# Optimization experiments

Hardware: AMD Instinct MI355X
Metric: run time of the kernel (lower is better)

## Reference

```python
import jax, jax.numpy as jnp
import numpy as np

D_MODEL = 1024
DEPTH = 1024

def setup_inputs() -> dict:
    key = jax.random.key(0)
    ks = jax.random.split(key, 7)
    scale = 1.0 / np.sqrt(D_MODEL)
    x = jax.random.normal(ks[0], (4, 2048, D_MODEL), dtype=jnp.float32)
    Wq = jax.random.normal(ks[1], (D_MODEL, DEPTH), dtype=jnp.float32) * scale
    Wk = jax.random.normal(ks[2], (D_MODEL, DEPTH), dtype=jnp.float32) * scale
    Wv = jax.random.normal(ks[3], (D_MODEL, DEPTH), dtype=jnp.float32) * scale
    bq = jnp.zeros((DEPTH,), dtype=jnp.float32)
    bk = jnp.zeros((DEPTH,), dtype=jnp.float32)
    bv = jnp.zeros((DEPTH,), dtype=jnp.float32)
    return {"x": x, "Wq": Wq, "bq": bq, "Wk": Wk, "bk": bk, "Wv": Wv, "bv": bv}

def reference(x, Wq, bq, Wk, bk, Wv, bv):
    # Q/K/V linear projections (Keras Dense: x @ W + b)
    q = jnp.einsum('bsd,de->bse', x, Wq) + bq  # [B,S,depth]
    k = jnp.einsum('bsd,de->bse', x, Wk) + bk
    v = jnp.einsum('bsd,de->bse', x, Wv) + bv
    d_k = jnp.asarray(q.shape[-1], dtype=q.dtype)
    scores = jnp.einsum('bse,bte->bst', q, k) / jnp.sqrt(d_k)  # [B,S,S]
    attn = jax.nn.softmax(scores, axis=-1)
    return jnp.einsum('bst,bte->bse', attn, v)  # [B,S,depth]
```

## Files before the change

kernel.cpp:

```cpp
#include <hip/hip_runtime.h>
#include <stdint.h>
#include <type_traits>

typedef unsigned short u16;
using short8  = __attribute__((ext_vector_type(8))) short;
using floatx4 = __attribute__((ext_vector_type(4))) float;

#define IC(n) (std::integral_constant<int, (n)>())

__device__ __forceinline__ u16 f2bf(float f) {
    unsigned u = __float_as_uint(f);
    u += 0x7fff + ((u >> 16) & 1);
    return (u16)(u >> 16);
}
__device__ __forceinline__ float bf2f(u16 h) {
    return __uint_as_float(((unsigned)h) << 16);
}

__device__ __forceinline__ void gload_lds16(const void* g, void* l) {
    auto gp = reinterpret_cast<const __attribute__((address_space(1))) unsigned int*>(
        reinterpret_cast<uintptr_t>(g));
    auto lp = reinterpret_cast<__attribute__((address_space(3))) unsigned int*>(
        reinterpret_cast<uintptr_t>(l));
    __builtin_amdgcn_global_load_lds(gp, lp, 16, 0, 0);
}

__global__ __launch_bounds__(256) void cvt_f32_bf16_kernel(
        const float* __restrict__ in, u16* __restrict__ out) {
    long i = ((long)blockIdx.x * 256 + threadIdx.x) * 4;
    float4 v = *(const float4*)(in + i);
    ushort4 o;
    o.x = f2bf(v.x); o.y = f2bf(v.y); o.z = f2bf(v.z); o.w = f2bf(v.w);
    *(ushort4*)(out + i) = o;
}

__global__ __launch_bounds__(256) void wt_kernel(
        const float* __restrict__ W0, const float* __restrict__ W1, const float* __restrict__ W2,
        u16* __restrict__ O0, u16* __restrict__ O1, u16* __restrict__ O2) {
    const float* W = blockIdx.z == 0 ? W0 : blockIdx.z == 1 ? W1 : W2;
    u16* O = blockIdx.z == 0 ? O0 : blockIdx.z == 1 ? O1 : O2;
    __shared__ float t[32][33];
    const int cx = threadIdx.x & 31, ry = threadIdx.x >> 5;
    const int d0 = blockIdx.x * 32, e0 = blockIdx.y * 32;
#pragma unroll
    for (int i = 0; i < 4; i++) t[ry + i * 8][cx] = W[(long)(d0 + ry + i * 8) * 1024 + e0 + cx];
    __syncthreads();
#pragma unroll
    for (int i = 0; i < 4; i++) O[(long)(e0 + ry + i * 8) * 1024 + d0 + cx] = f2bf(t[cx][ry + i * 8]);
}

__global__ __launch_bounds__(256) void vt_kernel(
        const u16* __restrict__ V, u16* __restrict__ Vt) {
    const int b = blockIdx.z;
    const u16* v = V + (long)b * 2048 * 1024;
    u16* o = Vt + (long)b * 1024 * 2048;
    __shared__ u16 t[32][33];
    const int cx = threadIdx.x & 31, ry = threadIdx.x >> 5;
    const int e0 = blockIdx.x * 32, t0 = blockIdx.y * 32;
#pragma unroll
    for (int i = 0; i < 4; i++) t[ry + i * 8][cx] = v[(long)(t0 + ry + i * 8) * 1024 + e0 + cx];
    __syncthreads();
#pragma unroll
    for (int i = 0; i < 4; i++) o[(long)(e0 + ry + i * 8) * 2048 + t0 + cx] = t[cx][ry + i * 8];
}

template <int MODE, int BNT>
__global__ __launch_bounds__(512) void gemm8_kernel(
        const u16* __restrict__ A, const u16* __restrict__ Bt,
        void* __restrict__ out0, void* __restrict__ out1, void* __restrict__ out2,
        const float* __restrict__ b0, const float* __restrict__ b1, const float* __restrict__ b2,
        int K, int N, long sAb, long sBb, long sCb, float scale)
{
    extern __shared__ u16 lds[];
    constexpr int DB   = (BNT == 256) ? 32768 : 24576;
    constexpr int FNH  = (BNT == 256) ? 2 : 1;
    constexpr int WCOL = (BNT == 256) ? 64 : 32;
    const int tid = threadIdx.x, lane = tid & 63, wid = tid >> 6;
    const int wm = wid >> 2, wn = wid & 3;
    const int l15 = lane & 15, hib = (lane >> 4) * 16;

    const int nbx = gridDim.x;
    const int nwg = nbx * gridDim.y;
    int lin = blockIdx.y * nbx + blockIdx.x;
    lin = (lin & 7) * (nwg >> 3) + (lin >> 3);
    const long m0 = (long)(lin / nbx) * 256;
    const long n0 = (long)(lin % nbx) * BNT;

    const u16* Ab = A + (long)blockIdx.z * sAb;
    const u16* Bb = Bt + (long)blockIdx.z * sBb;
    const long ldk = K;
    const int NT = K >> 6;

    auto stA = [&](int dbuf, int S, int kt) {
#pragma unroll
        for (int i = 0; i < 2; ++i) {
            const int rl = tid >> 3;
            const int R  = S * 64 + rl;
            const int cb = (tid & 7) * 16;
            const int scb = cb ^ ((R & 7) << 4);
            const u16* src = Ab + (m0 + i * 128 + R) * ldk + (long)kt * 64 + (scb >> 1);
            u16* dst = lds + dbuf * DB + i * 8192 + S * 4096 + wid * 512;
            gload_lds16(src, dst);
        }
    };
    auto stB = [&](int dbuf, int NHs, int kt) {
#pragma unroll
        for (int i = 0; i < 2; ++i) {
            const int c = i * 2 + (wid >> 2);
            const int h = c >> 1, rb = (c & 1) * 64;
            const int w = (wid & 3) * 64 + lane;
            const int r32 = w >> 3;
            const int R = rb + NHs * 32 + r32;
            const int cb = (w & 7) * 16;
            const int scb = cb ^ ((R & 7) << 4);
            const u16* src = Bb + (n0 + h * 128 + R) * ldk + (long)kt * 64 + (scb >> 1);
            u16* dst = lds + dbuf * DB + 16384 + h * 8192 + (rb + NHs * 32) * 64 + (wid & 3) * 512;
            gload_lds16(src, dst);
        }
    };
    auto stB128 = [&](int dbuf, int kt) {
#pragma unroll
        for (int i = 0; i < 2; ++i) {
            const int R = i * 64 + (tid >> 3);
            const int cb = (tid & 7) * 16;
            const int scb = cb ^ ((R & 7) << 4);
            const u16* src = Bb + (n0 + R) * ldk + (long)kt * 64 + (scb >> 1);
            u16* dst = lds + dbuf * DB + 16384 + i * 4096 + tid * 8;
            gload_lds16(src, dst);
        }
    };

    floatx4 acc[8][2 * FNH] = {};
    short8 afr[4][2], bfr[FNH][2];

    auto LA = [&](int dbuf, auto MHc) {
        constexpr int MH = decltype(MHc)::value;
        const char* reg = (const char*)(lds + dbuf * DB + wm * 8192);
#pragma unroll
        for (int fm = 0; fm < 4; ++fm)
#pragma unroll
            for (int ks = 0; ks < 2; ++ks) {
                const int r = MH * 64 + fm * 16 + l15;
                const int cb = ks * 64 + hib;
                afr[fm][ks] = *(const short8*)(reg + r * 128 + (cb ^ ((r & 7) << 4)));
            }
    };
    auto LB = [&](int dbuf, auto NHc) {
        constexpr int NH = decltype(NHc)::value;
        if constexpr (BNT == 256) {
            const char* reg = (const char*)(lds + dbuf * DB + 16384 + (wn >> 1) * 8192);
#pragma unroll
            for (int fn = 0; fn < 2; ++fn)
#pragma unroll
                for (int ks = 0; ks < 2; ++ks) {
                    const int r = (wn & 1) * 64 + NH * 32 + fn * 16 + l15;
                    const int cb = ks * 64 + hib;
                    bfr[fn][ks] = *(const short8*)(reg + r * 128 + (cb ^ ((r & 7) << 4)));
                }
        } else {
            const char* reg = (const char*)(lds + dbuf * DB + 16384);
#pragma unroll
            for (int ks = 0; ks < 2; ++ks) {
                const int r = wn * 32 + NH * 16 + l15;
                const int cb = ks * 64 + hib;
                bfr[0][ks] = *(const short8*)(reg + r * 128 + (cb ^ ((r & 7) << 4)));
            }
        }
    };
    auto MM = [&](auto MHc, auto NHc) {
        constexpr int MH = decltype(MHc)::value;
        constexpr int NH = decltype(NHc)::value;
        __builtin_amdgcn_s_setprio(1);
#pragma unroll
        for (int fm = 0; fm < 4; ++fm)
#pragma unroll
            for (int fn = 0; fn < FNH; ++fn)
#pragma unroll
                for (int ks = 0; ks < 2; ++ks)
                    acc[MH * 4 + fm][NH * FNH + fn] = __builtin_amdgcn_mfma_f32_16x16x32_bf16(
                        afr[fm][ks], bfr[fn][ks], acc[MH * 4 + fm][NH * FNH + fn], 0, 0, 0);
        __builtin_amdgcn_s_setprio(0);
    };

#define BAR()   __builtin_amdgcn_s_barrier()
#define WAIT0() asm volatile("s_waitcnt lgkmcnt(0)" ::: "memory")

    if constexpr (BNT == 256) {
        stA(0, 0, 0); stA(0, 1, 0); stB(0, 0, 0); stB(0, 1, 0);
        stA(1, 0, 1); stB(1, 1, 1); stA(1, 1, 1);
        asm volatile("s_waitcnt vmcnt(6)");
    } else {
        stA(0, 0, 0); stA(0, 1, 0); stB128(0, 0);
        stA(1, 0, 1); stA(1, 1, 1);
        asm volatile("s_waitcnt vmcnt(4)");
    }
    BAR();

    auto pair = [&](auto LASTC, int kt0) {
        constexpr bool L = decltype(LASTC)::value;
        if constexpr (BNT == 256) {
            LA(0, IC(0)); LB(0, IC(0));
            stB(1, 0, kt0 + 1);
            asm volatile("s_waitcnt lgkmcnt(8)");
            BAR(); WAIT0(); MM(IC(0), IC(0)); BAR();
            LB(0, IC(1));
            if (!L) stA(0, 0, kt0 + 2);
            BAR(); WAIT0(); MM(IC(0), IC(1)); BAR();
            LA(0, IC(1));
            if (!L) stB(0, 1, kt0 + 2);
            BAR(); WAIT0(); MM(IC(1), IC(1)); BAR();
            LB(0, IC(0));
            if (!L) stA(0, 1, kt0 + 2);
            BAR(); WAIT0(); MM(IC(1), IC(0));
            if (L) asm volatile("s_waitcnt vmcnt(0)");
            else   asm volatile("s_waitcnt vmcnt(6)");
            BAR();
            LA(1, IC(0)); LB(1, IC(0));
            if (!L) stB(0, 0, kt0 + 2);
            asm volatile("s_waitcnt lgkmcnt(8)");
            BAR(); WAIT0(); MM(IC(0), IC(0)); BAR();
            LB(1, IC(1));
            if (!L) stA(1, 0, kt0 + 3);
            BAR(); WAIT0(); MM(IC(0), IC(1)); BAR();
            LA(1, IC(1));
            if (!L) stB(1, 1, kt0 + 3);
            BAR(); WAIT0(); MM(IC(1), IC(1)); BAR();
            LB(1, IC(0));
            if (!L) stA(1, 1, kt0 + 3);
            BAR(); WAIT0(); MM(IC(1), IC(0));
            if (L) asm volatile("s_waitcnt vmcnt(0)");
            else   asm volatile("s_waitcnt vmcnt(6)");
            BAR();
        } else {
            LA(0, IC(0)); LB(0, IC(0));
            stB128(1, kt0 + 1);
            asm volatile("s_waitcnt lgkmcnt(8)");
            BAR(); WAIT0(); MM(IC(0), IC(0)); BAR();
            LB(0, IC(1));
            if (!L) stA(0, 0, kt0 + 2);
            BAR(); WAIT0(); MM(IC(0), IC(1)); BAR();
            LA(0, IC(1));
            if (!L) stA(0, 1, kt0 + 2);
            BAR(); WAIT0(); MM(IC(1), IC(1)); BAR();
            LB(0, IC(0));
            BAR(); WAIT0(); MM(IC(1), IC(0));
            if (L) asm volatile("s_waitcnt vmcnt(0)");
            else   asm volatile("s_waitcnt vmcnt(4)");
            BAR();
            LA(1, IC(0)); LB(1, IC(0));
            if (!L) stB128(0, kt0 + 2);
            asm volatile("s_waitcnt lgkmcnt(8)");
            BAR(); WAIT0(); MM(IC(0), IC(0)); BAR();
            LB(1, IC(1));
            if (!L) stA(1, 0, kt0 + 3);
            BAR(); WAIT0(); MM(IC(0), IC(1)); BAR();
            LA(1, IC(1));
            if (!L) stA(1, 1, kt0 + 3);
            BAR(); WAIT0(); MM(IC(1), IC(1)); BAR();
            LB(1, IC(0));
            BAR(); WAIT0(); MM(IC(1), IC(0));
            if (L) asm volatile("s_waitcnt vmcnt(0)");
            else   asm volatile("s_waitcnt vmcnt(4)");
            BAR();
        }
    };

    const int NITER = NT >> 1;
    int it = 0;
    for (; it < NITER - 1; ++it) pair(std::false_type{}, 2 * it);
    pair(std::true_type{}, 2 * it);

#undef BAR
#undef WAIT0

    const int cr = (lane >> 4) * 4, cc = l15;
    if (MODE == 0) {
        const int sel = (int)(n0 >> 10);
        u16* O = (u16*)(sel == 0 ? out0 : sel == 1 ? out1 : out2);
        const float* bias = sel == 0 ? b0 : sel == 1 ? b1 : b2;
        const long nc0 = n0 & 1023;
#pragma unroll
        for (int an = 0; an < 2 * FNH; ++an) {
            const long col = nc0 + wn * WCOL + an * 16 + cc;
            const float bvv = bias[col];
#pragma unroll
            for (int am = 0; am < 8; ++am) {
                const long row = m0 + wm * 128 + am * 16 + cr;
#pragma unroll
                for (int j = 0; j < 4; ++j)
                    O[(row + j) * 1024 + col] = f2bf(acc[am][an][j] + bvv);
            }
        }
    } else {
#pragma unroll
        for (int an = 0; an < 2 * FNH; ++an) {
            const long col = n0 + wn * WCOL + an * 16 + cc;
#pragma unroll
            for (int am = 0; am < 8; ++am) {
                const long row = m0 + wm * 128 + am * 16 + cr;
#pragma unroll
                for (int j = 0; j < 4; ++j) {
                    const long idx = (long)blockIdx.z * sCb + (row + j) * (long)N + col;
                    if (MODE == 1) ((u16*)out0)[idx] = f2bf(acc[am][an][j] * scale);
                    else           ((float*)out0)[idx] = acc[am][an][j];
                }
            }
        }
    }
}

__global__ __launch_bounds__(256) void softmax_kernel(u16* __restrict__ S) {
    u16* p = S + (long)blockIdx.x * 2048;
    const int tid = threadIdx.x;
    union { int4 q; u16 u[8]; } in;
    in.q = *(const int4*)(p + tid * 8);
    float v[8];
#pragma unroll
    for (int i = 0; i < 8; i++) v[i] = bf2f(in.u[i]);
    float mx = v[0];
#pragma unroll
    for (int i = 1; i < 8; i++) mx = fmaxf(mx, v[i]);
#pragma unroll
    for (int off = 32; off; off >>= 1) mx = fmaxf(mx, __shfl_xor(mx, off));
    __shared__ float red[8];
    if ((tid & 63) == 0) red[tid >> 6] = mx;
    __syncthreads();
    mx = fmaxf(fmaxf(red[0], red[1]), fmaxf(red[2], red[3]));
    float s = 0.f;
#pragma unroll
    for (int i = 0; i < 8; i++) { v[i] = __expf(v[i] - mx); s += v[i]; }
#pragma unroll
    for (int off = 32; off; off >>= 1) s += __shfl_xor(s, off);
    if ((tid & 63) == 0) red[4 + (tid >> 6)] = s;
    __syncthreads();
    s = red[4] + red[5] + red[6] + red[7];
    const float inv = 1.f / s;
    union { int4 q; u16 u[8]; } out;
#pragma unroll
    for (int i = 0; i < 8; i++) out.u[i] = f2bf(v[i] * inv);
    *(int4*)(p + tid * 8) = out.q;
}

extern "C" void kernel_launch(void* const* d_in, const int* in_sizes, int n_in,
                              void* d_out, int out_size, void* d_ws, size_t ws_size,
                              hipStream_t stream) {
    const float* x  = (const float*)d_in[0];
    const float* Wq = (const float*)d_in[1];
    const float* bq = (const float*)d_in[2];
    const float* Wk = (const float*)d_in[3];
    const float* bk = (const float*)d_in[4];
    const float* Wv = (const float*)d_in[5];
    const float* bv = (const float*)d_in[6];
    float* out = (float*)d_out;

    char* ws = (char*)d_ws;
    const long MB = 1L << 20;
    u16* xb = (u16*)(ws);
    u16* wt = (u16*)(ws + 16 * MB);
    u16* Q  = (u16*)(ws + 22 * MB);
    u16* Kb = (u16*)(ws + 38 * MB);
    u16* Vb = (u16*)(ws + 54 * MB);
    u16* Vt = (u16*)(ws + 70 * MB);
    u16* Sc = (u16*)(ws + 86 * MB);

    (void)hipFuncSetAttribute((const void*)gemm8_kernel<0, 256>, hipFuncAttributeMaxDynamicSharedMemorySize, 131072);
    (void)hipFuncSetAttribute((const void*)gemm8_kernel<1, 256>, hipFuncAttributeMaxDynamicSharedMemorySize, 131072);
    (void)hipFuncSetAttribute((const void*)gemm8_kernel<2, 128>, hipFuncAttributeMaxDynamicSharedMemorySize, 131072);

    cvt_f32_bf16_kernel<<<8192, 256, 0, stream>>>(x, xb);
    wt_kernel<<<dim3(32, 32, 3), 256, 0, stream>>>(Wq, Wk, Wv, wt, wt + 1024 * 1024, wt + 2 * 1024 * 1024);
    gemm8_kernel<0, 256><<<dim3(12, 32, 1), 512, 131072, stream>>>(
        xb, wt, Q, Kb, Vb, bq, bk, bv, 1024, 3072, 0, 0, 0, 1.f);
    vt_kernel<<<dim3(32, 64, 4), 256, 0, stream>>>(Vb, Vt);
    gemm8_kernel<1, 256><<<dim3(8, 8, 4), 512, 131072, stream>>>(
        Q, Kb, Sc, nullptr, nullptr, nullptr, nullptr, nullptr,
        1024, 2048, 2048L * 1024, 2048L * 1024, 2048L * 2048, 0.03125f);
    softmax_kernel<<<8192, 256, 0, stream>>>(Sc);
    gemm8_kernel<2, 128><<<dim3(8, 8, 4), 512, 98304, stream>>>(
        Sc, Vt, out, nullptr, nullptr, nullptr, nullptr, nullptr,
        2048, 1024, 2048L * 2048, 1024L * 2048, 2048L * 1024, 1.f);
}
```

Baseline: 184.1 us.

## Interleave LDS fragment loads with MFMA phases and drop explicit lgkmcnt waits

Within each barrier-delimited phase of the GEMM main loop, the LDS reads for the next A/B fragments now follow the MFMA block directly, before the closing barrier. Previously they were issued after that barrier, followed by a manual `lgkmcnt` wait. The global-to-LDS prefetch for the next buffer is also issued before the first fragment loads. The explicit `s_waitcnt lgkmcnt` calls are removed, so the compiler's own dependency waits handle LDS read completion. The goal is to hide LDS latency behind matrix-core work, at the risk that compiler-placed waits serialize differently or lengthen register live ranges.

```diff
diff --git a/kernel.cpp b/kernel.cpp
--- a/kernel.cpp
+++ b/kernel.cpp
@@ -182,8 +182,7 @@
         __builtin_amdgcn_s_setprio(0);
     };
 
-#define BAR()   __builtin_amdgcn_s_barrier()
-#define WAIT0() asm volatile("s_waitcnt lgkmcnt(0)" ::: "memory")
+#define BAR() __builtin_amdgcn_s_barrier()
 
     if constexpr (BNT == 256) {
         stA(0, 0, 0); stA(0, 1, 0); stB(0, 0, 0); stB(0, 1, 0);
@@ -199,66 +198,50 @@
     auto pair = [&](auto LASTC, int kt0) {
         constexpr bool L = decltype(LASTC)::value;
         if constexpr (BNT == 256) {
+            stB(1, 0, kt0 + 1);
             LA(0, IC(0)); LB(0, IC(0));
-            stB(1, 0, kt0 + 1);
-            asm volatile("s_waitcnt lgkmcnt(8)");
-            BAR(); WAIT0(); MM(IC(0), IC(0)); BAR();
-            LB(0, IC(1));
+            BAR(); MM(IC(0), IC(0)); LB(0, IC(1)); BAR();
             if (!L) stA(0, 0, kt0 + 2);
-            BAR(); WAIT0(); MM(IC(0), IC(1)); BAR();
-            LA(0, IC(1));
+            BAR(); MM(IC(0), IC(1)); LA(0, IC(1)); BAR();
             if (!L) stB(0, 1, kt0 + 2);
-            BAR(); WAIT0(); MM(IC(1), IC(1)); BAR();
-            LB(0, IC(0));
+            BAR(); MM(IC(1), IC(1)); LB(0, IC(0)); BAR();
             if (!L) stA(0, 1, kt0 + 2);
-            BAR(); WAIT0(); MM(IC(1), IC(0));
+            BAR(); MM(IC(1), IC(0));
             if (L) asm volatile("s_waitcnt vmcnt(0)");
             else   asm volatile("s_waitcnt vmcnt(6)");
             BAR();
+            if (!L) stB(0, 0, kt0 + 2);
             LA(1, IC(0)); LB(1, IC(0));
-            if (!L) stB(0, 0, kt0 + 2);
-            asm volatile("s_waitcnt lgkmcnt(8)");
-            BAR(); WAIT0(); MM(IC(0), IC(0)); BAR();
-            LB(1, IC(1));
+            BAR(); MM(IC(0), IC(0)); LB(1, IC(1)); BAR();
             if (!L) stA(1, 0, kt0 + 3);
-            BAR(); WAIT0(); MM(IC(0), IC(1)); BAR();
-            LA(1, IC(1));
+            BAR(); MM(IC(0), IC(1)); LA(1, IC(1)); BAR();
             if (!L) stB(1, 1, kt0 + 3);
-            BAR(); WAIT0(); MM(IC(1), IC(1)); BAR();
-            LB(1, IC(0));
+            BAR(); MM(IC(1), IC(1)); LB(1, IC(0)); BAR();
             if (!L) stA(1, 1, kt0 + 3);
-            BAR(); WAIT0(); MM(IC(1), IC(0));
+            BAR(); MM(IC(1), IC(0));
             if (L) asm volatile("s_waitcnt vmcnt(0)");
             else   asm volatile("s_waitcnt vmcnt(6)");
             BAR();
         } else {
+            stB128(1, kt0 + 1);
             LA(0, IC(0)); LB(0, IC(0));
-            stB128(1, kt0 + 1);
-            asm volatile("s_waitcnt lgkmcnt(8)");
-            BAR(); WAIT0(); MM(IC(0), IC(0)); BAR();
-            LB(0, IC(1));
+            BAR(); MM(IC(0), IC(0)); LB(0, IC(1)); BAR();
             if (!L) stA(0, 0, kt0 + 2);
-            BAR(); WAIT0(); MM(IC(0), IC(1)); BAR();
-            LA(0, IC(1));
+            BAR(); MM(IC(0), IC(1)); LA(0, IC(1)); BAR();
             if (!L) stA(0, 1, kt0 + 2);
-            BAR(); WAIT0(); MM(IC(1), IC(1)); BAR();
-            LB(0, IC(0));
-            BAR(); WAIT0(); MM(IC(1), IC(0));
+            BAR(); MM(IC(1), IC(1)); LB(0, IC(0)); BAR();
+            BAR(); MM(IC(1), IC(0));
             if (L) asm volatile("s_waitcnt vmcnt(0)");
             else   asm volatile("s_waitcnt vmcnt(4)");
             BAR();
+            if (!L) stB128(0, kt0 + 2);
             LA(1, IC(0)); LB(1, IC(0));
-            if (!L) stB128(0, kt0 + 2);
-            asm volatile("s_waitcnt lgkmcnt(8)");
-            BAR(); WAIT0(); MM(IC(0), IC(0)); BAR();
-            LB(1, IC(1));
+            BAR(); MM(IC(0), IC(0)); LB(1, IC(1)); BAR();
             if (!L) stA(1, 0, kt0 + 3);
-            BAR(); WAIT0(); MM(IC(0), IC(1)); BAR();
-            LA(1, IC(1));
+            BAR(); MM(IC(0), IC(1)); LA(1, IC(1)); BAR();
             if (!L) stA(1, 1, kt0 + 3);
-            BAR(); WAIT0(); MM(IC(1), IC(1)); BAR();
-            LB(1, IC(0));
-            BAR(); WAIT0(); MM(IC(1), IC(0));
+            BAR(); MM(IC(1), IC(1)); LB(1, IC(0)); BAR();
+            BAR(); MM(IC(1), IC(0));
             if (L) asm volatile("s_waitcnt vmcnt(0)");
             else   asm volatile("s_waitcnt vmcnt(4)");
             BAR();
@@ -271,7 +254,6 @@
     pair(std::true_type{}, 2 * it);
 
 #undef BAR
-#undef WAIT0
 
     const int cr = (lane >> 4) * 4, cc = l15;
     if (MODE == 0) {
```

Result: no change. 181.9 us (-1.2%).

## Restructure GEMM main-loop barriers/prefetch schedule and vectorize V transpose

Applied to the files above, without the earlier changes.

The GEMM inner pipeline is reorganized: explicit lgkmcnt waits and most per-MMA barrier pairs are dropped, and global-to-LDS prefetches are regrouped into paired issues fenced by barriers, with vmcnt thresholds adjusted to match. This is meant to cut synchronization stalls between LDS fragment loads and MFMA phases. Separately, the V transpose kernel moves to 64x64 tiles with 4-wide vector loads and stores. Removing the explicit lgkmcnt waits relies on the compiler to insert the right waits before MFMAs, and the changed prefetch placement risks LDS buffer overwrite races if the barriers no longer cover every hazard.

```diff
diff --git a/kernel.cpp b/kernel.cpp
--- a/kernel.cpp
+++ b/kernel.cpp
@@ -54,14 +54,21 @@
     const int b = blockIdx.z;
     const u16* v = V + (long)b * 2048 * 1024;
     u16* o = Vt + (long)b * 1024 * 2048;
-    __shared__ u16 t[32][33];
-    const int cx = threadIdx.x & 31, ry = threadIdx.x >> 5;
-    const int e0 = blockIdx.x * 32, t0 = blockIdx.y * 32;
-#pragma unroll
-    for (int i = 0; i < 4; i++) t[ry + i * 8][cx] = v[(long)(t0 + ry + i * 8) * 1024 + e0 + cx];
+    __shared__ u16 t[64][68];
+    const int c4 = (threadIdx.x & 15) * 4, r = threadIdx.x >> 4;
+    const int e0 = blockIdx.x * 64, t0 = blockIdx.y * 64;
+#pragma unroll
+    for (int i = 0; i < 4; i++)
+        *(ushort4*)&t[r + i * 16][c4] =
+            *(const ushort4*)(v + (long)(t0 + r + i * 16) * 1024 + e0 + c4);
     __syncthreads();
 #pragma unroll
-    for (int i = 0; i < 4; i++) o[(long)(e0 + ry + i * 8) * 2048 + t0 + cx] = t[cx][ry + i * 8];
+    for (int i = 0; i < 4; i++) {
+        const int e = r + i * 16;
+        ushort4 d;
+        d.x = t[c4 + 0][e]; d.y = t[c4 + 1][e]; d.z = t[c4 + 2][e]; d.w = t[c4 + 3][e];
+        *(ushort4*)(o + (long)(e0 + e) * 2048 + t0 + c4) = d;
+    }
 }
 
 template <int MODE, int BNT>
@@ -182,85 +189,86 @@
         __builtin_amdgcn_s_setprio(0);
     };
 
-#define BAR()   __builtin_amdgcn_s_barrier()
-#define WAIT0() asm volatile("s_waitcnt lgkmcnt(0)" ::: "memory")
+#define BAR() __builtin_amdgcn_s_barrier()
 
     if constexpr (BNT == 256) {
         stA(0, 0, 0); stA(0, 1, 0); stB(0, 0, 0); stB(0, 1, 0);
-        stA(1, 0, 1); stB(1, 1, 1); stA(1, 1, 1);
-        asm volatile("s_waitcnt vmcnt(6)");
+        stA(1, 0, 1); stB(1, 1, 1);
+        asm volatile("s_waitcnt vmcnt(4)");
     } else {
         stA(0, 0, 0); stA(0, 1, 0); stB128(0, 0);
-        stA(1, 0, 1); stA(1, 1, 1);
-        asm volatile("s_waitcnt vmcnt(4)");
+        stA(1, 0, 1);
+        asm volatile("s_waitcnt vmcnt(2)");
     }
     BAR();
 
     auto pair = [&](auto LASTC, int kt0) {
         constexpr bool L = decltype(LASTC)::value;
         if constexpr (BNT == 256) {
+            stA(1, 1, kt0 + 1); stB(1, 0, kt0 + 1);
             LA(0, IC(0)); LB(0, IC(0));
-            stB(1, 0, kt0 + 1);
-            asm volatile("s_waitcnt lgkmcnt(8)");
-            BAR(); WAIT0(); MM(IC(0), IC(0)); BAR();
+            BAR();
+            MM(IC(0), IC(0));
             LB(0, IC(1));
-            if (!L) stA(0, 0, kt0 + 2);
-            BAR(); WAIT0(); MM(IC(0), IC(1)); BAR();
+            MM(IC(0), IC(1));
             LA(0, IC(1));
-            if (!L) stB(0, 1, kt0 + 2);
-            BAR(); WAIT0(); MM(IC(1), IC(1)); BAR();
+            BAR();
+            if (!L) { stA(0, 0, kt0 + 2); stB(0, 1, kt0 + 2); }
+            BAR();
+            MM(IC(1), IC(1));
             LB(0, IC(0));
-            if (!L) stA(0, 1, kt0 + 2);
-            BAR(); WAIT0(); MM(IC(1), IC(0));
-            if (L) asm volatile("s_waitcnt vmcnt(0)");
-            else   asm volatile("s_waitcnt vmcnt(6)");
-            BAR();
-            LA(1, IC(0)); LB(1, IC(0));
-            if (!L) stB(0, 0, kt0 + 2);
-            asm volatile("s_waitcnt lgkmcnt(8)");
-            BAR(); WAIT0(); MM(IC(0), IC(0)); BAR();
-            LB(1, IC(1));
-            if (!L) stA(1, 0, kt0 + 3);
-            BAR(); WAIT0(); MM(IC(0), IC(1)); BAR();
-            LA(1, IC(1));
-            if (!L) stB(1, 1, kt0 + 3);
-            BAR(); WAIT0(); MM(IC(1), IC(1)); BAR();
-            LB(1, IC(0));
-            if (!L) stA(1, 1, kt0 + 3);
-            BAR(); WAIT0(); MM(IC(1), IC(0));
-            if (L) asm volatile("s_waitcnt vmcnt(0)");
-            else   asm volatile("s_waitcnt vmcnt(6)");
-            BAR();
-        } else {
-            LA(0, IC(0)); LB(0, IC(0));
-            stB128(1, kt0 + 1);
-            asm volatile("s_waitcnt lgkmcnt(8)");
-            BAR(); WAIT0(); MM(IC(0), IC(0)); BAR();
-            LB(0, IC(1));
-            if (!L) stA(0, 0, kt0 + 2);
-            BAR(); WAIT0(); MM(IC(0), IC(1)); BAR();
-            LA(0, IC(1));
-            if (!L) stA(0, 1, kt0 + 2);
-            BAR(); WAIT0(); MM(IC(1), IC(1)); BAR();
-            LB(0, IC(0));
-            BAR(); WAIT0(); MM(IC(1), IC(0));
+            MM(IC(1), IC(0));
             if (L) asm volatile("s_waitcnt vmcnt(0)");
             else   asm volatile("s_waitcnt vmcnt(4)");
             BAR();
+            if (!L) { stA(0, 1, kt0 + 2); stB(0, 0, kt0 + 2); }
             LA(1, IC(0)); LB(1, IC(0));
-            if (!L) stB128(0, kt0 + 2);
-            asm volatile("s_waitcnt lgkmcnt(8)");
-            BAR(); WAIT0(); MM(IC(0), IC(0)); BAR();
+            BAR();
+            MM(IC(0), IC(0));
             LB(1, IC(1));
-            if (!L) stA(1, 0, kt0 + 3);
-            BAR(); WAIT0(); MM(IC(0), IC(1)); BAR();
+            MM(IC(0), IC(1));
             LA(1, IC(1));
-            if (!L) stA(1, 1, kt0 + 3);
-            BAR(); WAIT0(); MM(IC(1), IC(1)); BAR();
+            BAR();
+            if (!L) { stA(1, 0, kt0 + 3); stB(1, 1, kt0 + 3); }
+            BAR();
+            MM(IC(1), IC(1));
             LB(1, IC(0));
-            BAR(); WAIT0(); MM(IC(1), IC(0));
+            MM(IC(1), IC(0));
             if (L) asm volatile("s_waitcnt vmcnt(0)");
             else   asm volatile("s_waitcnt vmcnt(4)");
+            BAR();
+        } else {
+            stA(1, 1, kt0 + 1); stB128(1, kt0 + 1);
+            LA(0, IC(0)); LB(0, IC(0));
+            BAR();
+            MM(IC(0), IC(0));
+            LB(0, IC(1));
+            MM(IC(0), IC(1));
+            LA(0, IC(1));
+            BAR();
+            if (!L) stA(0, 0, kt0 + 2);
+            BAR();
+            MM(IC(1), IC(1));
+            LB(0, IC(0));
+            MM(IC(1), IC(0));
+            if (L) asm volatile("s_waitcnt vmcnt(0)");
+            else   asm volatile("s_waitcnt vmcnt(2)");
+            BAR();
+            if (!L) { stA(0, 1, kt0 + 2); stB128(0, kt0 + 2); }
+            LA(1, IC(0)); LB(1, IC(0));
+            BAR();
+            MM(IC(0), IC(0));
+            LB(1, IC(1));
+            MM(IC(0), IC(1));
+            LA(1, IC(1));
+            BAR();
+            if (!L) stA(1, 0, kt0 + 3);
+            BAR();
+            MM(IC(1), IC(1));
+            LB(1, IC(0));
+            MM(IC(1), IC(0));
+            if (L) asm volatile("s_waitcnt vmcnt(0)");
+            else   asm volatile("s_waitcnt vmcnt(2)");
             BAR();
         }
     };
@@ -271,7 +279,6 @@
     pair(std::true_type{}, 2 * it);
 
 #undef BAR
-#undef WAIT0
 
     const int cr = (lane >> 4) * 4, cc = l15;
     if (MODE == 0) {
@@ -371,7 +378,7 @@
     wt_kernel<<<dim3(32, 32, 3), 256, 0, stream>>>(Wq, Wk, Wv, wt, wt + 1024 * 1024, wt + 2 * 1024 * 1024);
     gemm8_kernel<0, 256><<<dim3(12, 32, 1), 512, 131072, stream>>>(
         xb, wt, Q, Kb, Vb, bq, bk, bv, 1024, 3072, 0, 0, 0, 1.f);
-    vt_kernel<<<dim3(32, 64, 4), 256, 0, stream>>>(Vb, Vt);
+    vt_kernel<<<dim3(16, 32, 4), 256, 0, stream>>>(Vb, Vt);
     gemm8_kernel<1, 256><<<dim3(8, 8, 4), 512, 131072, stream>>>(
         Q, Kb, Sc, nullptr, nullptr, nullptr, nullptr, nullptr,
         1024, 2048, 2048L * 1024, 2048L * 1024, 2048L * 2048, 0.03125f);
```

Result: no change. 183.1 us (-0.5%).
